# Kernel optimization log

Measured on AMD Instinct MI355X. Metric: run time of the kernel, lower is better.

## Reference

```python
import jax, jax.numpy as jnp
import numpy as np
from jax import lax

WBITS = 2
ABITS = 2
STRIDES = (1, 1)
PADDING = 'SAME'


def _ste_quantize(x, k):
    # round(x * n) / n with straight-through gradient (identity)
    n = float(2 ** k - 1)
    q = jnp.round(x * n) / n
    return x + lax.stop_gradient(q - x)


def _quantize_weight(w, k):
    # DoReFa-style weight quantization: tanh, normalize to [0,1], quantize, map to [-1,1]
    t = jnp.tanh(w)
    t = t / jnp.max(jnp.abs(t)) * 0.5 + 0.5
    return 2.0 * _ste_quantize(t, k) - 1.0


def _quantize_act(x, k):
    return _ste_quantize(jnp.clip(x, 0.0, 1.0), k)


def setup_inputs() -> dict:
    key = jax.random.key(0)
    kx, kw = jax.random.split(key)
    x = jax.random.uniform(kx, (32, 56, 56, 256), dtype=jnp.float32)  # NHWC
    w = jax.random.normal(kw, (3, 3, 256, 256), dtype=jnp.float32) * 0.2  # HWIO
    # match init normalization: unit L2 norm per output channel over (h,w,cin)
    w = w / jnp.sqrt(1e-7 + jnp.sum(w * w, axis=(0, 1, 2), keepdims=True))
    return {'x': x, 'w': w}


def reference(x, w) -> jnp.ndarray:
    wq = _quantize_weight(w, WBITS)        # low-bit weights in [-1, 1]
    xq = _quantize_act(x, ABITS)           # low-bit activations in [0, 1]
    out = lax.conv_general_dilated(
        xq, wq,
        window_strides=STRIDES,
        padding=PADDING,
        dimension_numbers=('NHWC', 'HWIO', 'NHWC'),
    )
    return out
```

## Files before the change

### kernel.cpp

```cpp
#include <hip/hip_runtime.h>
#include <stdint.h>

#define GLOBAL_AS __attribute__((address_space(1)))
#define LDS_AS    __attribute__((address_space(3)))

typedef int   v4i  __attribute__((ext_vector_type(4)));
typedef int   v8i  __attribute__((ext_vector_type(8)));
typedef float v16f __attribute__((ext_vector_type(16)));

__device__ __forceinline__ void gload_lds16(const void* g, void* l) {
    __builtin_amdgcn_global_load_lds((GLOBAL_AS uint32_t*)g, (LDS_AS uint32_t*)l, 16, 0, 0);
}


__global__ void k_xq_wmax(const float* __restrict__ x, const float* __restrict__ w,
                          int8_t* __restrict__ xqp, unsigned* __restrict__ maxbits) {
    const int bid = blockIdx.x;
    if (bid < 48) {
        int t = bid * 256 + threadIdx.x;
        const float4* w4 = (const float4*)w;
        float m = 0.f;
        for (int i = t; i < 147456; i += 12288) {
            float4 v = w4[i];
            m = fmaxf(m, fmaxf(fmaxf(fabsf(tanhf(v.x)), fabsf(tanhf(v.y))),
                               fmaxf(fabsf(tanhf(v.z)), fabsf(tanhf(v.w)))));
        }
#pragma unroll
        for (int off = 32; off > 0; off >>= 1)
            m = fmaxf(m, __shfl_xor(m, off, 64));
        if ((threadIdx.x & 63) == 0) atomicMax(maxbits, __float_as_uint(m));
        return;
    }
    int t = (bid - 48) * 256 + threadIdx.x;
    int g  = t & 7;
    int p  = t >> 3;
    int xp = p % 58;
    int q  = p / 58;
    int yp = q % 58;
    int n  = q / 58;
    int4 r;
    if (yp == 0 || yp == 57 || xp == 0 || xp == 57) {
        r = make_int4(0, 0, 0, 0);
    } else {
        const float4* px = (const float4*)(x + (((long)((n * 56 + (yp - 1)) * 56 + (xp - 1))) << 8) + g * 32);
        int wds[4];
#pragma unroll
        for (int jj = 0; jj < 4; ++jj) {
            float4 v0 = px[jj * 2];
            float4 v1 = px[jj * 2 + 1];
            int q0 = (int)rintf(fminf(fmaxf(v0.x, 0.f), 1.f) * 3.f);
            int q1 = (int)rintf(fminf(fmaxf(v0.y, 0.f), 1.f) * 3.f);
            int q2 = (int)rintf(fminf(fmaxf(v0.z, 0.f), 1.f) * 3.f);
            int q3 = (int)rintf(fminf(fmaxf(v0.w, 0.f), 1.f) * 3.f);
            int q4 = (int)rintf(fminf(fmaxf(v1.x, 0.f), 1.f) * 3.f);
            int q5 = (int)rintf(fminf(fmaxf(v1.y, 0.f), 1.f) * 3.f);
            int q6 = (int)rintf(fminf(fmaxf(v1.z, 0.f), 1.f) * 3.f);
            int q7 = (int)rintf(fminf(fmaxf(v1.w, 0.f), 1.f) * 3.f);
            wds[jj] = ((0x5420 >> (q0 << 2)) & 0xF)        | (((0x5420 >> (q1 << 2)) & 0xF) << 4)
                    | (((0x5420 >> (q2 << 2)) & 0xF) << 8) | (((0x5420 >> (q3 << 2)) & 0xF) << 12)
                    | (((0x5420 >> (q4 << 2)) & 0xF) << 16)| (((0x5420 >> (q5 << 2)) & 0xF) << 20)
                    | (((0x5420 >> (q6 << 2)) & 0xF) << 24)| (((0x5420 >> (q7 << 2)) & 0xF) << 28);
        }
        r = make_int4(wds[0], wds[1], wds[2], wds[3]);
    }
    *(int4*)(xqp + ((long)t << 4)) = r;
}

__global__ void k_wq(const float* __restrict__ w, const unsigned* __restrict__ maxbits,
                     int8_t* __restrict__ wqt) {
    int t = blockIdx.x * 256 + threadIdx.x;
    int co = t & 255;
    int kblk = t >> 8;
    float inv = 0.5f / __uint_as_float(*maxbits);
    uint8_t b[16];
#pragma unroll
    for (int j = 0; j < 16; ++j) {
        float t0 = tanhf(w[(long)(kblk * 32 + 2 * j) * 256 + co]);
        float t1 = tanhf(w[(long)(kblk * 32 + 2 * j + 1) * 256 + co]);
        int q0 = (int)rintf((t0 * inv + 0.5f) * 3.0f);
        int q1 = (int)rintf((t1 * inv + 0.5f) * 3.0f);
        b[j] = (uint8_t)(((0x52AD >> (q0 << 2)) & 0xF) | (((0x52AD >> (q1 << 2)) & 0xF) << 4));
    }
    *(int4*)(wqt + (long)co * 1152 + kblk * 16) = *(int4*)b;
}

__global__ __launch_bounds__(256) void k_conv(const int8_t* __restrict__ xqp,
                                              const int8_t* __restrict__ wqt,
                                              float* __restrict__ out) {
    __shared__ int8_t sX[256 * 128];

    const int tid  = threadIdx.x;
    const int wv   = tid >> 6;
    const int lane = tid & 63;
    const int orig = blockIdx.x;
    const int work = (orig & 7) * 200 + (orig >> 3);
    const int coBase = (work & 1) << 7;
    const int wt   = work >> 1;
    const int n    = wt / 25;
    const int t    = wt - n * 25;

    const int m0 = t * 128;
    const int y0 = m0 / 56;
    const int x0 = m0 - y0 * 56;
    const long pixBase = ((long)(n * 58 + y0)) * 58 + x0;

    {
        const int lr = lane >> 3;
        const int lp = lane & 7;
#pragma unroll
        for (int j = 0; j < 8; ++j) {
            int p = wv * 8 + j * 32 + lr;
            int g = lp ^ (p & 7);
            long pg = pixBase + p;
            if (pg > 107647) pg = 107647;
            gload_lds16(xqp + (pg << 7) + g * 16, &sX[(wv * 8 + j * 32) * 128]);
        }
    }

    const int wm  = (wv & 1) * 64;
    const int wn  = (wv >> 1) * 64;
    const int l31 = lane & 31;
    const int hi  = lane >> 5;
    const int h16 = hi << 4;

    const int8_t* pB0 = wqt + (long)(coBase + wn + l31) * 1152 + h16;
    const int8_t* pB1 = pB0 + 32 * 1152;

    int mL0 = m0 + wm + l31;      if (mL0 > 3135) mL0 = 3135;
    int mL1 = m0 + wm + 32 + l31; if (mL1 > 3135) mL1 = 3135;
    const int yR0 = mL0 / 56, xR0 = mL0 - yR0 * 56;
    const int yR1 = mL1 / 56, xR1 = mL1 - yR1 * 56;
    const int po0 = (yR0 - y0) * 58 + (xR0 - x0);
    const int po1 = (yR1 - y0) * 58 + (xR1 - x0);

    v16f acc00 = {0,0,0,0,0,0,0,0,0,0,0,0,0,0,0,0};
    v16f acc01 = {0,0,0,0,0,0,0,0,0,0,0,0,0,0,0,0};
    v16f acc10 = {0,0,0,0,0,0,0,0,0,0,0,0,0,0,0,0};
    v16f acc11 = {0,0,0,0,0,0,0,0,0,0,0,0,0,0,0,0};

    __syncthreads();

    const int SC = 0x7F7F7F7F;

#define MFMA_KK(KK, B0K, B1K)                                                              \
    {                                                                                      \
        const int kc = (KK) * 32 + h16;                                                    \
        v4i a0 = *(const v4i*)(a0b + (kc ^ xx0));                                          \
        v4i a1 = *(const v4i*)(a1b + (kc ^ xx1));                                          \
        v8i A0 = {a0[0], a0[1], a0[2], a0[3], 0, 0, 0, 0};                                 \
        v8i A1 = {a1[0], a1[1], a1[2], a1[3], 0, 0, 0, 0};                                 \
        v8i B0 = {B0K[0], B0K[1], B0K[2], B0K[3], 0, 0, 0, 0};                             \
        v8i B1 = {B1K[0], B1K[1], B1K[2], B1K[3], 0, 0, 0, 0};                             \
        acc00 = __builtin_amdgcn_mfma_scale_f32_32x32x64_f8f6f4(A0, B0, acc00, 4, 4, 0, SC, 0, SC); \
        acc01 = __builtin_amdgcn_mfma_scale_f32_32x32x64_f8f6f4(A0, B1, acc01, 4, 4, 0, SC, 0, SC); \
        acc10 = __builtin_amdgcn_mfma_scale_f32_32x32x64_f8f6f4(A1, B0, acc10, 4, 4, 0, SC, 0, SC); \
        acc11 = __builtin_amdgcn_mfma_scale_f32_32x32x64_f8f6f4(A1, B1, acc11, 4, 4, 0, SC, 0, SC); \
    }

#pragma unroll
    for (int ky = 0; ky < 3; ++ky) {
#pragma unroll
        for (int kx = 0; kx < 3; ++kx) {
            const int it = ky * 3 + kx;
            const int8_t* pBt0 = pB0 + it * 128;
            const int8_t* pBt1 = pB1 + it * 128;
            v4i b0_0 = *(const v4i*)(pBt0);
            v4i b0_1 = *(const v4i*)(pBt0 + 32);
            v4i b0_2 = *(const v4i*)(pBt0 + 64);
            v4i b0_3 = *(const v4i*)(pBt0 + 96);
            v4i b1_0 = *(const v4i*)(pBt1);
            v4i b1_1 = *(const v4i*)(pBt1 + 32);
            v4i b1_2 = *(const v4i*)(pBt1 + 64);
            v4i b1_3 = *(const v4i*)(pBt1 + 96);
            const int pL0 = po0 + ky * 58 + kx;
            const int pL1 = po1 + ky * 58 + kx;
            const int8_t* a0b = sX + pL0 * 128;
            const int8_t* a1b = sX + pL1 * 128;
            const int xx0 = (pL0 & 7) << 4;
            const int xx1 = (pL1 & 7) << 4;
            __builtin_amdgcn_s_setprio(1);
            MFMA_KK(0, b0_0, b1_0)
            MFMA_KK(1, b0_1, b1_1)
            MFMA_KK(2, b0_2, b1_2)
            MFMA_KK(3, b0_3, b1_3)
            __builtin_amdgcn_s_setprio(0);
        }
    }
#undef MFMA_KK

    const float s = 1.0f / 9.0f;
    const long outImg = (long)n * 3136;

#define ST1(ACC, MT, REG)                                                                  \
    {                                                                                      \
        const int row = ((REG) & 3) + 8 * ((REG) >> 2) + 4 * hi;                           \
        const int rowLocal = m0 + wm + (MT) * 32 + row;                                    \
        if (rowLocal < 3136)                                                               \
            out[(outImg + rowLocal) * 256 + ocol] = ACC[REG] * s;                          \
    }
#define ST_ALL(ACC, MT, NT)                                                                \
    {                                                                                      \
        const int ocol = coBase + wn + (NT) * 32 + l31;                                    \
        ST1(ACC, MT, 0)  ST1(ACC, MT, 1)  ST1(ACC, MT, 2)  ST1(ACC, MT, 3)                 \
        ST1(ACC, MT, 4)  ST1(ACC, MT, 5)  ST1(ACC, MT, 6)  ST1(ACC, MT, 7)                 \
        ST1(ACC, MT, 8)  ST1(ACC, MT, 9)  ST1(ACC, MT, 10) ST1(ACC, MT, 11)                \
        ST1(ACC, MT, 12) ST1(ACC, MT, 13) ST1(ACC, MT, 14) ST1(ACC, MT, 15)                \
    }

    ST_ALL(acc00, 0, 0)
    ST_ALL(acc01, 0, 1)
    ST_ALL(acc10, 1, 0)
    ST_ALL(acc11, 1, 1)
#undef ST_ALL
#undef ST1
}

extern "C" void kernel_launch(void* const* d_in, const int* in_sizes, int n_in,
                              void* d_out, int out_size, void* d_ws, size_t ws_size,
                              hipStream_t stream) {
    const float* x = (const float*)d_in[0];
    const float* w = (const float*)d_in[1];
    float* out = (float*)d_out;

    unsigned* maxbits = (unsigned*)d_ws;
    int8_t* wqt = (int8_t*)d_ws + 4096;
    int8_t* xqp = (int8_t*)d_ws + 4096 + 294912;

    hipMemsetAsync(maxbits, 0, 4, stream);
    k_xq_wmax<<<48 + 3364, 256, 0, stream>>>(x, w, xqp, maxbits);
    k_wq<<<72, 256, 0, stream>>>(w, maxbits, wqt);
    k_conv<<<1600, 256, 0, stream>>>(xqp, wqt, out);
}
```

Before: 284.9 us.

## Stage weight tiles through double-buffered LDS with async global-to-LDS loads

Weights were previously read per wave straight from global memory into registers at each of the nine filter taps. They are now loaded cooperatively into a swizzled, double-buffered LDS tile with global_load_lds. The next tap's load is issued while the current tap computes, and stages are separated by vmcnt waits and barriers. This aims to hide weight-load latency and cut redundant global reads across waves, at the cost of 32KB more LDS (hurting occupancy) and two barriers per tap.

```diff
diff --git a/kernel.cpp b/kernel.cpp
--- a/kernel.cpp
+++ b/kernel.cpp
@@ -84,10 +84,14 @@
     *(int4*)(wqt + (long)co * 1152 + kblk * 16) = *(int4*)b;
 }
 
+#define BM 128
+#define BN 128
+
 __global__ __launch_bounds__(256) void k_conv(const int8_t* __restrict__ xqp,
                                               const int8_t* __restrict__ wqt,
                                               float* __restrict__ out) {
     __shared__ int8_t sX[256 * 128];
+    __shared__ int8_t sB[2][128 * 128];
 
     const int tid  = threadIdx.x;
     const int wv   = tid >> 6;
@@ -104,17 +108,24 @@
     const int x0 = m0 - y0 * 56;
     const long pixBase = ((long)(n * 58 + y0)) * 58 + x0;
 
-    {
-        const int lr = lane >> 3;
-        const int lp = lane & 7;
-#pragma unroll
-        for (int j = 0; j < 8; ++j) {
-            int p = wv * 8 + j * 32 + lr;
-            int g = lp ^ (p & 7);
-            long pg = pixBase + p;
-            if (pg > 107647) pg = 107647;
-            gload_lds16(xqp + (pg << 7) + g * 16, &sX[(wv * 8 + j * 32) * 128]);
-        }
+    const int lr = lane >> 3;
+    const int lp = lane & 7;
+
+#pragma unroll
+    for (int j = 0; j < 8; ++j) {
+        int p = wv * 8 + j * 32 + lr;
+        int g = lp ^ (p & 7);
+        long pg = pixBase + p;
+        if (pg > 107647) pg = 107647;
+        gload_lds16(xqp + (pg << 7) + g * 16, &sX[(wv * 8 + j * 32) * 128]);
+    }
+
+    const int8_t* bB[4];
+#pragma unroll
+    for (int j = 0; j < 4; ++j) {
+        int r = wv * 8 + j * 32 + lr;
+        int g = lp ^ (r & 7);
+        bB[j] = wqt + (long)(coBase + r) * 1152 + g * 16;
     }
 
     const int wm  = (wv & 1) * 64;
@@ -122,9 +133,6 @@
     const int l31 = lane & 31;
     const int hi  = lane >> 5;
     const int h16 = hi << 4;
-
-    const int8_t* pB0 = wqt + (long)(coBase + wn + l31) * 1152 + h16;
-    const int8_t* pB1 = pB0 + 32 * 1152;
 
     int mL0 = m0 + wm + l31;      if (mL0 > 3135) mL0 = 3135;
     int mL1 = m0 + wm + 32 + l31; if (mL1 > 3135) mL1 = 3135;
@@ -133,60 +141,67 @@
     const int po0 = (yR0 - y0) * 58 + (xR0 - x0);
     const int po1 = (yR1 - y0) * 58 + (xR1 - x0);
 
+    const int rB0 = (wn + l31) * 128;       const int bxr0 = ((wn + l31) & 7) << 4;
+    const int rB1 = (wn + 32 + l31) * 128;  const int bxr1 = ((wn + 32 + l31) & 7) << 4;
+
     v16f acc00 = {0,0,0,0,0,0,0,0,0,0,0,0,0,0,0,0};
     v16f acc01 = {0,0,0,0,0,0,0,0,0,0,0,0,0,0,0,0};
     v16f acc10 = {0,0,0,0,0,0,0,0,0,0,0,0,0,0,0,0};
     v16f acc11 = {0,0,0,0,0,0,0,0,0,0,0,0,0,0,0,0};
 
-    __syncthreads();
-
     const int SC = 0x7F7F7F7F;
 
-#define MFMA_KK(KK, B0K, B1K)                                                              \
-    {                                                                                      \
-        const int kc = (KK) * 32 + h16;                                                    \
-        v4i a0 = *(const v4i*)(a0b + (kc ^ xx0));                                          \
-        v4i a1 = *(const v4i*)(a1b + (kc ^ xx1));                                          \
-        v8i A0 = {a0[0], a0[1], a0[2], a0[3], 0, 0, 0, 0};                                 \
-        v8i A1 = {a1[0], a1[1], a1[2], a1[3], 0, 0, 0, 0};                                 \
-        v8i B0 = {B0K[0], B0K[1], B0K[2], B0K[3], 0, 0, 0, 0};                             \
-        v8i B1 = {B1K[0], B1K[1], B1K[2], B1K[3], 0, 0, 0, 0};                             \
-        acc00 = __builtin_amdgcn_mfma_scale_f32_32x32x64_f8f6f4(A0, B0, acc00, 4, 4, 0, SC, 0, SC); \
-        acc01 = __builtin_amdgcn_mfma_scale_f32_32x32x64_f8f6f4(A0, B1, acc01, 4, 4, 0, SC, 0, SC); \
-        acc10 = __builtin_amdgcn_mfma_scale_f32_32x32x64_f8f6f4(A1, B0, acc10, 4, 4, 0, SC, 0, SC); \
-        acc11 = __builtin_amdgcn_mfma_scale_f32_32x32x64_f8f6f4(A1, B1, acc11, 4, 4, 0, SC, 0, SC); \
-    }
-
-#pragma unroll
-    for (int ky = 0; ky < 3; ++ky) {
-#pragma unroll
-        for (int kx = 0; kx < 3; ++kx) {
-            const int it = ky * 3 + kx;
-            const int8_t* pBt0 = pB0 + it * 128;
-            const int8_t* pBt1 = pB1 + it * 128;
-            v4i b0_0 = *(const v4i*)(pBt0);
-            v4i b0_1 = *(const v4i*)(pBt0 + 32);
-            v4i b0_2 = *(const v4i*)(pBt0 + 64);
-            v4i b0_3 = *(const v4i*)(pBt0 + 96);
-            v4i b1_0 = *(const v4i*)(pBt1);
-            v4i b1_1 = *(const v4i*)(pBt1 + 32);
-            v4i b1_2 = *(const v4i*)(pBt1 + 64);
-            v4i b1_3 = *(const v4i*)(pBt1 + 96);
-            const int pL0 = po0 + ky * 58 + kx;
-            const int pL1 = po1 + ky * 58 + kx;
-            const int8_t* a0b = sX + pL0 * 128;
-            const int8_t* a1b = sX + pL1 * 128;
-            const int xx0 = (pL0 & 7) << 4;
-            const int xx1 = (pL1 & 7) << 4;
-            __builtin_amdgcn_s_setprio(1);
-            MFMA_KK(0, b0_0, b1_0)
-            MFMA_KK(1, b0_1, b1_1)
-            MFMA_KK(2, b0_2, b1_2)
-            MFMA_KK(3, b0_3, b1_3)
-            __builtin_amdgcn_s_setprio(0);
+    auto issueB = [&](int it, int b) {
+#pragma unroll
+        for (int j = 0; j < 4; ++j)
+            gload_lds16(bB[j] + it * 128, &sB[b][(wv * 8 + j * 32) * 128]);
+    };
+
+    auto compute = [&](int it, int b) {
+        const int tapoff = (it / 3) * 58 + (it % 3);
+        const int pL0 = po0 + tapoff;
+        const int pL1 = po1 + tapoff;
+        const int8_t* a0b = sX + pL0 * 128;
+        const int8_t* a1b = sX + pL1 * 128;
+        const int xx0 = (pL0 & 7) << 4;
+        const int xx1 = (pL1 & 7) << 4;
+        const int8_t* pB = sB[b];
+        __builtin_amdgcn_s_setprio(1);
+#pragma unroll
+        for (int kk = 0; kk < 4; ++kk) {
+            const int kc = kk * 32 + h16;
+            v4i a0 = *(const v4i*)(a0b + (kc ^ xx0));
+            v4i a1 = *(const v4i*)(a1b + (kc ^ xx1));
+            v4i b0 = *(const v4i*)(pB + rB0 + (kc ^ bxr0));
+            v4i b1 = *(const v4i*)(pB + rB1 + (kc ^ bxr1));
+            v8i A0 = {a0[0], a0[1], a0[2], a0[3], 0, 0, 0, 0};
+            v8i A1 = {a1[0], a1[1], a1[2], a1[3], 0, 0, 0, 0};
+            v8i B0 = {b0[0], b0[1], b0[2], b0[3], 0, 0, 0, 0};
+            v8i B1 = {b1[0], b1[1], b1[2], b1[3], 0, 0, 0, 0};
+            acc00 = __builtin_amdgcn_mfma_scale_f32_32x32x64_f8f6f4(A0, B0, acc00, 4, 4, 0, SC, 0, SC);
+            acc01 = __builtin_amdgcn_mfma_scale_f32_32x32x64_f8f6f4(A0, B1, acc01, 4, 4, 0, SC, 0, SC);
+            acc10 = __builtin_amdgcn_mfma_scale_f32_32x32x64_f8f6f4(A1, B0, acc10, 4, 4, 0, SC, 0, SC);
+            acc11 = __builtin_amdgcn_mfma_scale_f32_32x32x64_f8f6f4(A1, B1, acc11, 4, 4, 0, SC, 0, SC);
         }
-    }
-#undef MFMA_KK
+        __builtin_amdgcn_s_setprio(0);
+    };
+
+    issueB(0, 0);
+#pragma unroll 2
+    for (int it = 0; it < 8; ++it) {
+        issueB(it + 1, (it + 1) & 1);
+        asm volatile("s_waitcnt vmcnt(4)" ::: "memory");
+        __builtin_amdgcn_s_barrier();
+        asm volatile("" ::: "memory");
+        compute(it, it & 1);
+        asm volatile("" ::: "memory");
+        __builtin_amdgcn_s_barrier();
+        asm volatile("" ::: "memory");
+    }
+    asm volatile("s_waitcnt vmcnt(0)" ::: "memory");
+    __builtin_amdgcn_s_barrier();
+    asm volatile("" ::: "memory");
+    compute(8, 0);
 
     const float s = 1.0f / 9.0f;
     const long outImg = (long)n * 3136;
```

New measurement: 229.9 us. -19.3%, faster.
